# Kernel tuning notes

Hardware: AMD Instinct MI355X
Metric: run time of the kernel (lower is better)

Reference implementation:

```python
import jax, jax.numpy as jnp
import numpy as np

N, E = 50000, 800000
IN, HID, HEADS, OUT = 128, 32, 4, 64
NEG_SLOPE = 0.2
BN_EPS = 1e-5


def setup_inputs() -> dict:
    key = jax.random.key(0)
    ks = jax.random.split(key, 24)
    d1 = HID * HEADS  # 128
    def glorot(k, shape):
        fan = shape[0] + shape[-1]
        return jax.random.uniform(k, shape, jnp.float32, -1.0, 1.0) * jnp.sqrt(6.0 / fan)
    inp = {
        'x': jax.random.normal(ks[0], (N, IN), jnp.float32),
        'edge_index': jax.random.randint(ks[1], (2, E), 0, N, jnp.int64),
        # layer 1: in -> hid x heads
        'W1': glorot(ks[2], (IN, d1)),
        'as1': glorot(ks[3], (HEADS, HID)),
        'ad1': glorot(ks[4], (HEADS, HID)),
        'b1': jnp.zeros((d1,), jnp.float32),
        'g1': jnp.ones((d1,), jnp.float32),
        'be1': jnp.zeros((d1,), jnp.float32),
        # layer 2: d1 -> hid x heads
        'W2': glorot(ks[5], (d1, d1)),
        'as2': glorot(ks[6], (HEADS, HID)),
        'ad2': glorot(ks[7], (HEADS, HID)),
        'b2': jnp.zeros((d1,), jnp.float32),
        'g2': jnp.ones((d1,), jnp.float32),
        'be2': jnp.zeros((d1,), jnp.float32),
        # layer 3: d1 -> out, heads=1, concat=False
        'W3': glorot(ks[8], (d1, OUT)),
        'as3': glorot(ks[9], (1, OUT)),
        'ad3': glorot(ks[10], (1, OUT)),
        'b3': jnp.zeros((OUT,), jnp.float32),
        'g3': jnp.ones((OUT,), jnp.float32),
        'be3': jnp.zeros((OUT,), jnp.float32),
    }
    return inp


def gat_conv(x, src, dst, W, a_s, a_d, b, heads, ch, concat):
    n = x.shape[0]
    h = (x @ W).reshape(n, heads, ch)                       # [N,H,C]
    al_s = jnp.sum(h * a_s, axis=-1)                        # [N,H]
    al_d = jnp.sum(h * a_d, axis=-1)                        # [N,H]
    e = jax.nn.leaky_relu(al_s[src] + al_d[dst], NEG_SLOPE)  # [E,H]
    m = jax.ops.segment_max(e, dst, num_segments=n)
    m = jnp.where(jnp.isfinite(m), m, 0.0)
    ex = jnp.exp(e - m[dst])
    denom = jax.ops.segment_sum(ex, dst, num_segments=n)
    alpha = ex / (denom[dst] + 1e-16)                       # segment softmax
    out = jax.ops.segment_sum(h[src] * alpha[:, :, None], dst, num_segments=n)
    out = out.reshape(n, heads * ch) if concat else out.mean(axis=1)
    return out + b


def batch_norm(x, g, b):
    mu = x.mean(axis=0)
    var = x.var(axis=0)
    return (x - mu) * jax.lax.rsqrt(var + BN_EPS) * g + b


def reference(x, edge_index, W1, as1, ad1, b1, g1, be1,
              W2, as2, ad2, b2, g2, be2,
              W3, as3, ad3, b3, g3, be3):
    n = x.shape[0]
    loops = jnp.arange(n, dtype=edge_index.dtype)
    src = jnp.concatenate([edge_index[0], loops])  # add_self_loops=True
    dst = jnp.concatenate([edge_index[1], loops])
    h = gat_conv(x, src, dst, W1, as1, ad1, b1, HEADS, HID, True)
    h = jax.nn.elu(batch_norm(h, g1, be1))
    h = gat_conv(h, src, dst, W2, as2, ad2, b2, HEADS, HID, True)
    h = jax.nn.elu(batch_norm(h, g2, be2))
    h = gat_conv(h, src, dst, W3, as3, ad3, b3, 1, OUT, False)
    h = jax.nn.elu(batch_norm(h, g3, be3))
    return h
```

## Files before the change

### kernel.cpp

```cpp
#include <hip/hip_runtime.h>
#include <hip/hip_bf16.h>
#include <math.h>

#define NEG_SLOPE 0.2f
#define BN_EPS 1e-5f

using short8_t = __attribute__((ext_vector_type(8))) short;
using f32x4    = __attribute__((ext_vector_type(4))) float;

__device__ __forceinline__ unsigned short f2bf(float f) {
    unsigned int u = __float_as_uint(f);
    u += 0x7FFF + ((u >> 16) & 1);
    return (unsigned short)(u >> 16);
}
__device__ __forceinline__ float bf2f(unsigned short h) {
    return __uint_as_float(((unsigned int)h) << 16);
}


__device__ __forceinline__ void wfrag_one(const float* __restrict__ W,
                                          unsigned short* __restrict__ Wf,
                                          int idx, int D)
{
    int CS = D / 32;
    int i    = idx & 7;
    int lane = (idx >> 3) & 63;
    int f    = idx >> 9;
    int ks   = f & 3;
    int cs   = (f >> 2) % CS;
    int wc   = (f >> 2) / CS;
    int k = ks * 32 + ((lane >> 4) << 3) + i;
    int d = wc * (D / 2) + cs * 16 + (lane & 15);
    Wf[idx] = f2bf(W[k * D + d]);
}

__global__ void setup_all(const float* __restrict__ W1, const float* __restrict__ W2,
                          const float* __restrict__ W3,
                          unsigned short* __restrict__ wf1, unsigned short* __restrict__ wf2,
                          unsigned short* __restrict__ wf3,
                          int* __restrict__ count, int N)
{
    int total = 16384 + 16384 + 8192 + N;
    int st = gridDim.x * blockDim.x;
    for (int idx = blockIdx.x * blockDim.x + threadIdx.x; idx < total; idx += st) {
        if (idx < 16384)       wfrag_one(W1, wf1, idx, 128);
        else if (idx < 32768)  wfrag_one(W2, wf2, idx - 16384, 128);
        else if (idx < 40960)  wfrag_one(W3, wf3, idx - 32768, 64);
        else                   count[idx - 40960] = 0;
    }
}


__global__ void dst_count(const int* __restrict__ ei, int E, int N,
                          int* __restrict__ count, int* __restrict__ ord)
{
    long long total = (long long)E + N;
    long long st = (long long)gridDim.x * blockDim.x;
    for (long long e = (long long)blockIdx.x * blockDim.x + threadIdx.x; e < total; e += st) {
        int dt = (e < E) ? ei[E + e] : (int)(e - E);
        ord[e] = atomicAdd(&count[dt], 1);
    }
}

__global__ void block_sum(const int* __restrict__ count, int* __restrict__ bsum, int N)
{
    __shared__ int sh[256];
    int b = blockIdx.x, t = threadIdx.x;
    int base = b * 1024;
    int s = 0;
    for (int i = t; i < 1024; i += 256) {
        int j = base + i;
        if (j < N) s += count[j];
    }
    sh[t] = s;
    __syncthreads();
    for (int off = 128; off > 0; off >>= 1) {
        if (t < off) sh[t] += sh[t + off];
        __syncthreads();
    }
    if (t == 0) bsum[b] = sh[0];
}

__global__ void scan_bsum(int* __restrict__ bsum, int nb, int* __restrict__ rowptr, int N, int total)
{
    __shared__ int sh[256];
    int t = threadIdx.x;
    sh[t] = (t < nb) ? bsum[t] : 0;
    __syncthreads();
    for (int off = 1; off < 256; off <<= 1) {
        int u = (t >= off) ? sh[t - off] : 0;
        __syncthreads();
        sh[t] += u;
        __syncthreads();
    }
    if (t < nb) bsum[t] = (t == 0) ? 0 : sh[t - 1];
    if (t == 0) rowptr[N] = total;
}

__global__ void scan_final(const int* __restrict__ count, const int* __restrict__ boff,
                           int* __restrict__ rowptr, int N)
{
    __shared__ int sh[256];
    int b = blockIdx.x, t = threadIdx.x;
    int base = b * 1024 + t * 4;
    int c[4];
    int s = 0;
    #pragma unroll
    for (int i = 0; i < 4; ++i) {
        int j = base + i;
        c[i] = (j < N) ? count[j] : 0;
        s += c[i];
    }
    sh[t] = s;
    __syncthreads();
    for (int off = 1; off < 256; off <<= 1) {
        int u = (t >= off) ? sh[t - off] : 0;
        __syncthreads();
        sh[t] += u;
        __syncthreads();
    }
    int run = boff[b] + ((t == 0) ? 0 : sh[t - 1]);
    #pragma unroll
    for (int i = 0; i < 4; ++i) {
        int j = base + i;
        if (j < N) rowptr[j] = run;
        run += c[i];
    }
}

__global__ void csr_scatter(const int* __restrict__ ei, int E, int N,
                            const int* __restrict__ rowptr, const int* __restrict__ ord,
                            int* __restrict__ srcs)
{
    long long total = (long long)E + N;
    long long st = (long long)gridDim.x * blockDim.x;
    for (long long e = (long long)blockIdx.x * blockDim.x + threadIdx.x; e < total; e += st) {
        int s, dt;
        if (e < E) { s = ei[e]; dt = ei[E + e]; }
        else       { s = dt = (int)(e - E); }
        srcs[rowptr[dt] + ord[e]] = s;
    }
}


template<int D, int H, bool BN>
__global__ __launch_bounds__(256, 4) void gemm_mfma(
        const float* __restrict__ x, const unsigned short* __restrict__ Wf,
        const float* __restrict__ colstats, const float* __restrict__ g,
        const float* __restrict__ be,
        const float* __restrict__ a_s, const float* __restrict__ a_d,
        unsigned short* __restrict__ hbuf,
        float* __restrict__ als, float* __restrict__ ald,
        int N, float invN)
{
    constexpr int CS = D / 32;
    __shared__ unsigned short xs[32 * 136];
    __shared__ float affA[128], affB[128];
    __shared__ float red2[4][4][4][2];
    int tid = threadIdx.x, lane = tid & 63, w = tid >> 6;
    int wr = w >> 1, wc = w & 1;
    int n0 = blockIdx.x * 32;

    short8_t bfr[CS][4];
    #pragma unroll
    for (int cs = 0; cs < CS; ++cs)
        #pragma unroll
        for (int ks = 0; ks < 4; ++ks)
            bfr[cs][ks] = *(const short8_t*)(Wf + (((wc * CS + cs) * 4 + ks) << 9) + (lane << 3));

    if (BN) {
        if (tid < 128) {
            float cs_ = colstats[tid], cq = colstats[tid + 128];
            float mu = cs_ * invN;
            float var = cq * invN - mu * mu;
            float s = rsqrtf(var + BN_EPS) * g[tid];
            affA[tid] = s;
            affB[tid] = be[tid] - mu * s;
        }
        __syncthreads();
    }

    for (int jj = tid; jj < 32 * 32; jj += 256) {
        int r = jj >> 5, q = jj & 31;
        float4 v = make_float4(0.f, 0.f, 0.f, 0.f);
        if (n0 + r < N) v = *(const float4*)(x + (long long)(n0 + r) * 128 + q * 4);
        if (BN) {
            int c = q * 4;
            v.x = affA[c]     * v.x + affB[c];
            v.y = affA[c + 1] * v.y + affB[c + 1];
            v.z = affA[c + 2] * v.z + affB[c + 2];
            v.w = affA[c + 3] * v.w + affB[c + 3];
            v.x = (v.x > 0.f) ? v.x : expm1f(v.x);
            v.y = (v.y > 0.f) ? v.y : expm1f(v.y);
            v.z = (v.z > 0.f) ? v.z : expm1f(v.z);
            v.w = (v.w > 0.f) ? v.w : expm1f(v.w);
        }
        ushort4 o;
        o.x = f2bf(v.x); o.y = f2bf(v.y); o.z = f2bf(v.z); o.w = f2bf(v.w);
        *(ushort4*)(xs + r * 136 + q * 4) = o;
    }
    __syncthreads();

    f32x4 acc[CS];
    #pragma unroll
    for (int cs = 0; cs < CS; ++cs) acc[cs] = (f32x4){0.f, 0.f, 0.f, 0.f};

    #pragma unroll
    for (int ks = 0; ks < 4; ++ks) {
        short8_t a = *(const short8_t*)(xs + (wr * 16 + (lane & 15)) * 136
                                           + ks * 32 + ((lane >> 4) << 3));
        #pragma unroll
        for (int cs = 0; cs < CS; ++cs)
            acc[cs] = __builtin_amdgcn_mfma_f32_16x16x32_bf16(a, bfr[cs][ks], acc[cs], 0, 0, 0);
    }

    int mrow = wr * 16 + ((lane >> 4) << 2);
    int dcol = wc * (D / 2) + (lane & 15);
    #pragma unroll
    for (int cs = 0; cs < CS; ++cs)
        #pragma unroll
        for (int r = 0; r < 4; ++r) {
            int n = n0 + mrow + r;
            if (n < N) hbuf[(long long)n * D + dcol + cs * 16] = f2bf(acc[cs][r]);
        }

    int l15 = lane & 15;
    if (H == 4) {
        float ps[2][4], pd[2][4];
        #pragma unroll
        for (int ch = 0; ch < 2; ++ch) {
            int hh = wc * 2 + ch;
            #pragma unroll
            for (int r = 0; r < 4; ++r) { ps[ch][r] = 0.f; pd[ch][r] = 0.f; }
            #pragma unroll
            for (int k2 = 0; k2 < 2; ++k2) {
                int cs = ch * 2 + k2;
                int cih = k2 * 16 + l15;
                float as_v = a_s[hh * 32 + cih];
                float ad_v = a_d[hh * 32 + cih];
                #pragma unroll
                for (int r = 0; r < 4; ++r) {
                    ps[ch][r] += acc[cs][r] * as_v;
                    pd[ch][r] += acc[cs][r] * ad_v;
                }
            }
        }
        #pragma unroll
        for (int off = 1; off < 16; off <<= 1)
            #pragma unroll
            for (int ch = 0; ch < 2; ++ch)
                #pragma unroll
                for (int r = 0; r < 4; ++r) {
                    ps[ch][r] += __shfl_xor(ps[ch][r], off);
                    pd[ch][r] += __shfl_xor(pd[ch][r], off);
                }
        if (l15 == 0) {
            #pragma unroll
            for (int r = 0; r < 4; ++r) {
                int n = n0 + mrow + r;
                if (n < N) {
                    #pragma unroll
                    for (int ch = 0; ch < 2; ++ch) {
                        als[(long long)n * 4 + wc * 2 + ch] = ps[ch][r];
                        ald[(long long)n * 4 + wc * 2 + ch] = pd[ch][r];
                    }
                }
            }
        }
    } else {
        float ps[4], pd[4];
        #pragma unroll
        for (int r = 0; r < 4; ++r) { ps[r] = 0.f; pd[r] = 0.f; }
        #pragma unroll
        for (int cs = 0; cs < CS; ++cs) {
            int c = wc * 32 + cs * 16 + l15;
            float as_v = a_s[c], ad_v = a_d[c];
            #pragma unroll
            for (int r = 0; r < 4; ++r) {
                ps[r] += acc[cs][r] * as_v;
                pd[r] += acc[cs][r] * ad_v;
            }
        }
        #pragma unroll
        for (int off = 1; off < 16; off <<= 1)
            #pragma unroll
            for (int r = 0; r < 4; ++r) {
                ps[r] += __shfl_xor(ps[r], off);
                pd[r] += __shfl_xor(pd[r], off);
            }
        int q = lane >> 4;
        if (l15 == 0) {
            #pragma unroll
            for (int r = 0; r < 4; ++r) {
                red2[w][q][r][0] = ps[r];
                red2[w][q][r][1] = pd[r];
            }
        }
        __syncthreads();
        if (tid < 64) {
            int wr2 = tid >> 5, row = (tid >> 1) & 15, sd = tid & 1;
            int qq = row >> 2, rr = row & 3;
            float v = red2[wr2 * 2][qq][rr][sd] + red2[wr2 * 2 + 1][qq][rr][sd];
            int n = n0 + wr2 * 16 + row;
            if (n < N) { if (sd) ald[n] = v; else als[n] = v; }
        }
    }
}

template<int H, int C>
__global__ __launch_bounds__(256) void gat_aggregate_v5(
        const int* __restrict__ rowptr, const int* __restrict__ srcs,
        const float* __restrict__ als, const float* __restrict__ ald,
        const unsigned short* __restrict__ hbuf, float* __restrict__ agg,
        float* __restrict__ part, int N)
{
    constexpr int D = H * C;
    constexpr int TPN = D / 8;
    constexpr int NPB = 256 / TPN;
    __shared__ float red[4][TPN * 16];
    int tid = threadIdx.x;
    int g = tid / TPN, l = tid % TPN;
    int n = blockIdx.x * NPB + g;
    bool active = (n < N);
    int c0 = l * 8;
    int hh = c0 / C;
    float aldv = active ? ald[(long long)n * H + hh] : 0.f;
    int beg = 0, end = 0;
    if (active) { beg = rowptr[n]; end = rowptr[n + 1]; }

    float wsum = 0.f;
    float acc[8];
    #pragma unroll
    for (int i = 0; i < 8; ++i) acc[i] = 0.f;

    int e = beg;
    for (; e + 4 <= end; e += 4) {
        int s0 = srcs[e], s1 = srcs[e + 1], s2 = srcs[e + 2], s3 = srcs[e + 3];
        float v0 = als[(long long)s0 * H + hh] + aldv;
        float v1 = als[(long long)s1 * H + hh] + aldv;
        float v2 = als[(long long)s2 * H + hh] + aldv;
        float v3 = als[(long long)s3 * H + hh] + aldv;
        v0 = (v0 >= 0.f) ? v0 : NEG_SLOPE * v0;
        v1 = (v1 >= 0.f) ? v1 : NEG_SLOPE * v1;
        v2 = (v2 >= 0.f) ? v2 : NEG_SLOPE * v2;
        v3 = (v3 >= 0.f) ? v3 : NEG_SLOPE * v3;
        float w0 = __expf(v0), w1 = __expf(v1), w2 = __expf(v2), w3 = __expf(v3);
        float4 q0 = *(const float4*)(hbuf + (long long)s0 * D + c0);
        float4 q1 = *(const float4*)(hbuf + (long long)s1 * D + c0);
        float4 q2 = *(const float4*)(hbuf + (long long)s2 * D + c0);
        float4 q3 = *(const float4*)(hbuf + (long long)s3 * D + c0);
        wsum += w0 + w1 + w2 + w3;
        const float* qf0 = (const float*)&q0;
        const float* qf1 = (const float*)&q1;
        const float* qf2 = (const float*)&q2;
        const float* qf3 = (const float*)&q3;
        #pragma unroll
        for (int i = 0; i < 4; ++i) {
            unsigned int u0 = __float_as_uint(qf0[i]);
            unsigned int u1 = __float_as_uint(qf1[i]);
            unsigned int u2 = __float_as_uint(qf2[i]);
            unsigned int u3 = __float_as_uint(qf3[i]);
            acc[2*i]   += w0 * __uint_as_float(u0 << 16)
                        + w1 * __uint_as_float(u1 << 16)
                        + w2 * __uint_as_float(u2 << 16)
                        + w3 * __uint_as_float(u3 << 16);
            acc[2*i+1] += w0 * __uint_as_float(u0 & 0xFFFF0000u)
                        + w1 * __uint_as_float(u1 & 0xFFFF0000u)
                        + w2 * __uint_as_float(u2 & 0xFFFF0000u)
                        + w3 * __uint_as_float(u3 & 0xFFFF0000u);
        }
    }
    for (; e < end; ++e) {
        int s = srcs[e];
        float v = als[(long long)s * H + hh] + aldv;
        v = (v >= 0.f) ? v : NEG_SLOPE * v;
        float w = __expf(v);
        float4 q = *(const float4*)(hbuf + (long long)s * D + c0);
        const float* qf = (const float*)&q;
        wsum += w;
        #pragma unroll
        for (int i = 0; i < 4; ++i) {
            unsigned int u = __float_as_uint(qf[i]);
            acc[2*i]   += w * __uint_as_float(u << 16);
            acc[2*i+1] += w * __uint_as_float(u & 0xFFFF0000u);
        }
    }
    float inv = active ? 1.f / (wsum + 1e-16f) : 0.f;
    float sv[16];
    #pragma unroll
    for (int i = 0; i < 8; ++i) {
        float o = acc[i] * inv;
        sv[i] = o;
        sv[8 + i] = o * o;
        acc[i] = o;
    }
    if (active) {
        *(float4*)(agg + (long long)n * D + c0)     = make_float4(acc[0], acc[1], acc[2], acc[3]);
        *(float4*)(agg + (long long)n * D + c0 + 4) = make_float4(acc[4], acc[5], acc[6], acc[7]);
    }

    #pragma unroll
    for (int off = TPN; off < 64; off <<= 1)
        #pragma unroll
        for (int j = 0; j < 16; ++j)
            sv[j] += __shfl_xor(sv[j], off);

    int w4 = tid >> 6, lane = tid & 63;
    if (lane < TPN) {
        #pragma unroll
        for (int j = 0; j < 16; ++j) red[w4][lane * 16 + j] = sv[j];
    }
    __syncthreads();
    if (w4 == 0 && lane < TPN) {
        #pragma unroll
        for (int ww = 1; ww < 4; ++ww)
            #pragma unroll
            for (int j = 0; j < 16; ++j) sv[j] += red[ww][lane * 16 + j];
        float* p = part + (long long)blockIdx.x * (2 * D) + lane * 16;
        *(float4*)(p)      = make_float4(sv[0],  sv[1],  sv[2],  sv[3]);
        *(float4*)(p + 4)  = make_float4(sv[4],  sv[5],  sv[6],  sv[7]);
        *(float4*)(p + 8)  = make_float4(sv[8],  sv[9],  sv[10], sv[11]);
        *(float4*)(p + 12) = make_float4(sv[12], sv[13], sv[14], sv[15]);
    }
}

template<int D>
__global__ __launch_bounds__(256) void reduce_stats(
        const float* __restrict__ part, int nblk, float* __restrict__ colsum)
{
    __shared__ float sh[256];
    int f = blockIdx.x;
    int t = threadIdx.x;
    int col = (f < D) ? f : (f - D);
    int off = (col / 8) * 16 + (col % 8) + ((f < D) ? 0 : 8);
    float s = 0.f;
    for (int i = t; i < nblk; i += 256)
        s += part[(long long)i * (2 * D) + off];
    sh[t] = s;
    __syncthreads();
    for (int o = 128; o > 0; o >>= 1) {
        if (t < o) sh[t] += sh[t + o];
        __syncthreads();
    }
    if (t == 0) colsum[(f < D) ? f : (128 + f - D)] = sh[0];
}

template<int D>
__global__ __launch_bounds__(256) void bn_apply_v2(
        const float* __restrict__ agg, const float* __restrict__ colsum,
        const float* __restrict__ g, const float* __restrict__ be,
        float* __restrict__ out, int N, float invN)
{
    constexpr int TPR = D / 4;
    constexpr int RPB = 256 / TPR;
    __shared__ float affA[D], affB[D];
    int tid = threadIdx.x;
    if (tid < D) {
        float mu = colsum[tid] * invN;
        float var = colsum[128 + tid] * invN - mu * mu;
        float s = rsqrtf(var + BN_EPS) * g[tid];
        affA[tid] = s;
        affB[tid] = be[tid] - mu * s;
    }
    __syncthreads();
    int rg = tid / TPR, cl = tid % TPR;
    int c = cl * 4;
    float a0 = affA[c], a1 = affA[c+1], a2 = affA[c+2], a3 = affA[c+3];
    float b0 = affB[c], b1 = affB[c+1], b2 = affB[c+2], b3 = affB[c+3];
    for (int r = blockIdx.x * RPB + rg; r < N; r += gridDim.x * RPB) {
        float4 v = *(const float4*)(agg + (long long)r * D + c);
        v.x = a0 * v.x + b0; v.y = a1 * v.y + b1;
        v.z = a2 * v.z + b2; v.w = a3 * v.w + b3;
        v.x = (v.x > 0.f) ? v.x : expm1f(v.x);
        v.y = (v.y > 0.f) ? v.y : expm1f(v.y);
        v.z = (v.z > 0.f) ? v.z : expm1f(v.z);
        v.w = (v.w > 0.f) ? v.w : expm1f(v.w);
        *(float4*)(out + (long long)r * D + c) = v;
    }
}

template<int H, int C, bool BN>
static void run_layer(const float* xin, int N,
                      const int* rowptr, const int* srcs,
                      const unsigned short* Wf, const float* a_s, const float* a_d,
                      const float* prev_stats, const float* prev_g, const float* prev_be,
                      unsigned short* hbuf, float* als, float* ald,
                      float* part, float* stats_out, float* agg,
                      hipStream_t stream)
{
    constexpr int D = H * C;
    constexpr int NPB = 256 / (D / 8);
    int nblk = (N + NPB - 1) / NPB;
    float invN = 1.f / (float)N;
    gemm_mfma<D, H, BN><<<(N + 31) / 32, 256, 0, stream>>>(
        xin, Wf, prev_stats, prev_g, prev_be, a_s, a_d, hbuf, als, ald, N, invN);
    gat_aggregate_v5<H, C><<<nblk, 256, 0, stream>>>(
        rowptr, srcs, als, ald, hbuf, agg, part, N);
    reduce_stats<D><<<2 * D, 256, 0, stream>>>(part, nblk, stats_out);
}

extern "C" void kernel_launch(void* const* d_in, const int* in_sizes, int n_in,
                              void* d_out, int out_size, void* d_ws, size_t ws_size,
                              hipStream_t stream)
{
    const float* x   = (const float*)d_in[0];
    const int*   ei  = (const int*)d_in[1];
    const float* W1  = (const float*)d_in[2];
    const float* as1 = (const float*)d_in[3];
    const float* ad1 = (const float*)d_in[4];
    const float* g1  = (const float*)d_in[6];
    const float* be1 = (const float*)d_in[7];
    const float* W2  = (const float*)d_in[8];
    const float* as2 = (const float*)d_in[9];
    const float* ad2 = (const float*)d_in[10];
    const float* g2  = (const float*)d_in[12];
    const float* be2 = (const float*)d_in[13];
    const float* W3  = (const float*)d_in[14];
    const float* as3 = (const float*)d_in[15];
    const float* ad3 = (const float*)d_in[16];
    const float* g3  = (const float*)d_in[18];
    const float* be3 = (const float*)d_in[19];

    const int N = in_sizes[0] / 128;
    const int E = in_sizes[1] / 2;
    const int NB = (N + 1023) / 1024;

    float* ws   = (float*)d_ws;
    float* aggA = ws;
    float* aggB = aggA + (long long)N * 128;
    float* als  = aggB + (long long)N * 128;
    float* ald  = als  + (long long)N * 4;
    float* cs0  = ald  + (long long)N * 4;
    float* cs1  = cs0 + 256;
    float* cs2  = cs1 + 256;
    unsigned short* hbuf = (unsigned short*)(cs2 + 256);
    int*   rowptr = (int*)(hbuf + (long long)N * 128);
    int*   count  = rowptr + (N + 1);
    int*   bsum   = count + N;
    int*   ord    = bsum + 256;
    int*   srcs   = ord + ((long long)E + N);
    unsigned short* wf1 = (unsigned short*)(srcs + ((long long)E + N));
    unsigned short* wf2 = wf1 + 128 * 128;
    unsigned short* wf3 = wf2 + 128 * 128;
    float* part = (float*)(wf3 + 128 * 64);

    setup_all<<<356, 256, 0, stream>>>(W1, W2, W3, wf1, wf2, wf3, count, N);

    dst_count<<<2048, 256, 0, stream>>>(ei, E, N, count, ord);
    block_sum<<<NB, 256, 0, stream>>>(count, bsum, N);
    scan_bsum<<<1, 256, 0, stream>>>(bsum, NB, rowptr, N, E + N);
    scan_final<<<NB, 256, 0, stream>>>(count, bsum, rowptr, N);
    csr_scatter<<<2048, 256, 0, stream>>>(ei, E, N, rowptr, ord, srcs);

    run_layer<4, 32, false>(x, N, rowptr, srcs, wf1, as1, ad1,
                            nullptr, nullptr, nullptr,
                            hbuf, als, ald, part, cs0, aggA, stream);
    run_layer<4, 32, true>(aggA, N, rowptr, srcs, wf2, as2, ad2,
                           cs0, g1, be1,
                           hbuf, als, ald, part, cs1, aggB, stream);
    run_layer<1, 64, true>(aggB, N, rowptr, srcs, wf3, as3, ad3,
                           cs1, g2, be2,
                           hbuf, als, ald, part, cs2, aggA, stream);
    bn_apply_v2<64><<<2048, 256, 0, stream>>>(aggA, cs2, g3, be3, (float*)d_out, N, 1.f / (float)N);
}
```

Baseline: 227.3 us.

## Sort destination nodes by degree to balance aggregation workload per block

Adds a counting-sort pass (histogram, scan, scatter) that builds a permutation of nodes ordered by in-degree, and makes the aggregation kernel process nodes via this permutation. Nodes with similar degree then share a block, which is meant to reduce intra-block imbalance and wavefront divergence in the edge loop. In exchange it adds three small kernel launches, an extra indirection per node, and scattered (non-contiguous) writes of agg rows and node reads.

```diff
diff --git a/kernel.cpp b/kernel.cpp
--- a/kernel.cpp
+++ b/kernel.cpp
@@ -4,6 +4,7 @@
 
 #define NEG_SLOPE 0.2f
 #define BN_EPS 1e-5f
+#define NBH 64
 
 using short8_t = __attribute__((ext_vector_type(8))) short;
 using f32x4    = __attribute__((ext_vector_type(4))) float;
@@ -139,6 +140,62 @@
         if (e < E) { s = ei[e]; dt = ei[E + e]; }
         else       { s = dt = (int)(e - E); }
         srcs[rowptr[dt] + ord[e]] = s;
+    }
+}
+
+
+__global__ void deg_hist(const int* __restrict__ count, int N, int chunk,
+                         int* __restrict__ hist)
+{
+    __shared__ int h[256];
+    int b = blockIdx.x, t = threadIdx.x;
+    h[t] = 0;
+    __syncthreads();
+    int lo = b * chunk, hi = min(N, lo + chunk);
+    for (int i = lo + t; i < hi; i += 256) {
+        int d = count[i]; if (d > 255) d = 255;
+        atomicAdd(&h[d], 1);
+    }
+    __syncthreads();
+    hist[b * 256 + t] = h[t];
+}
+
+__global__ void deg_scan(const int* __restrict__ hist, int* __restrict__ blockBase)
+{
+    __shared__ int tot[256];
+    int t = threadIdx.x;
+    int s = 0;
+    for (int b = 0; b < NBH; ++b) s += hist[b * 256 + t];
+    int v = s;
+    tot[t] = s;
+    __syncthreads();
+    for (int off = 1; off < 256; off <<= 1) {
+        int u = (t >= off) ? tot[t - off] : 0;
+        __syncthreads();
+        tot[t] += u;
+        __syncthreads();
+    }
+    int run = tot[t] - v;
+    for (int b = 0; b < NBH; ++b) {
+        blockBase[b * 256 + t] = run;
+        run += hist[b * 256 + t];
+    }
+}
+
+__global__ void perm_scatter(const int* __restrict__ count, int N, int chunk,
+                             const int* __restrict__ blockBase, int* __restrict__ perm)
+{
+    __shared__ int h[256];
+    __shared__ int bb[256];
+    int b = blockIdx.x, t = threadIdx.x;
+    h[t] = 0;
+    bb[t] = blockBase[b * 256 + t];
+    __syncthreads();
+    int lo = b * chunk, hi = min(N, lo + chunk);
+    for (int i = lo + t; i < hi; i += 256) {
+        int d = count[i]; if (d > 255) d = 255;
+        int lr = atomicAdd(&h[d], 1);
+        perm[bb[d] + lr] = i;
     }
 }
 
@@ -308,7 +365,8 @@
 }
 
 template<int H, int C>
-__global__ __launch_bounds__(256) void gat_aggregate_v5(
+__global__ __launch_bounds__(256) void gat_aggregate_v6(
+        const int* __restrict__ perm,
         const int* __restrict__ rowptr, const int* __restrict__ srcs,
         const float* __restrict__ als, const float* __restrict__ ald,
         const unsigned short* __restrict__ hbuf, float* __restrict__ agg,
@@ -320,8 +378,9 @@
     __shared__ float red[4][TPN * 16];
     int tid = threadIdx.x;
     int g = tid / TPN, l = tid % TPN;
-    int n = blockIdx.x * NPB + g;
-    bool active = (n < N);
+    int idx = blockIdx.x * NPB + g;
+    bool active = (idx < N);
+    int n = active ? perm[idx] : 0;
     int c0 = l * 8;
     int hh = c0 / C;
     float aldv = active ? ald[(long long)n * H + hh] : 0.f;
@@ -481,7 +540,7 @@
 
 template<int H, int C, bool BN>
 static void run_layer(const float* xin, int N,
-                      const int* rowptr, const int* srcs,
+                      const int* perm, const int* rowptr, const int* srcs,
                       const unsigned short* Wf, const float* a_s, const float* a_d,
                       const float* prev_stats, const float* prev_g, const float* prev_be,
                       unsigned short* hbuf, float* als, float* ald,
@@ -494,8 +553,8 @@
     float invN = 1.f / (float)N;
     gemm_mfma<D, H, BN><<<(N + 31) / 32, 256, 0, stream>>>(
         xin, Wf, prev_stats, prev_g, prev_be, a_s, a_d, hbuf, als, ald, N, invN);
-    gat_aggregate_v5<H, C><<<nblk, 256, 0, stream>>>(
-        rowptr, srcs, als, ald, hbuf, agg, part, N);
+    gat_aggregate_v6<H, C><<<nblk, 256, 0, stream>>>(
+        perm, rowptr, srcs, als, ald, hbuf, agg, part, N);
     reduce_stats<D><<<2 * D, 256, 0, stream>>>(part, nblk, stats_out);
 }
 
@@ -524,6 +583,7 @@
     const int N = in_sizes[0] / 128;
     const int E = in_sizes[1] / 2;
     const int NB = (N + 1023) / 1024;
+    const int CHUNK = (N + NBH - 1) / NBH;
 
     float* ws   = (float*)d_ws;
     float* aggA = ws;
@@ -543,6 +603,9 @@
     unsigned short* wf2 = wf1 + 128 * 128;
     unsigned short* wf3 = wf2 + 128 * 128;
     float* part = (float*)(wf3 + 128 * 64);
+    int*   hist = (int*)(part + ((long long)(N + 15) / 16) * 256);
+    int*   bbase = hist + NBH * 256;
+    int*   perm  = bbase + NBH * 256;
 
     setup_all<<<356, 256, 0, stream>>>(W1, W2, W3, wf1, wf2, wf3, count, N);
 
@@ -552,13 +615,17 @@
     scan_final<<<NB, 256, 0, stream>>>(count, bsum, rowptr, N);
     csr_scatter<<<2048, 256, 0, stream>>>(ei, E, N, rowptr, ord, srcs);
 
-    run_layer<4, 32, false>(x, N, rowptr, srcs, wf1, as1, ad1,
+    deg_hist<<<NBH, 256, 0, stream>>>(count, N, CHUNK, hist);
+    deg_scan<<<1, 256, 0, stream>>>(hist, bbase);
+    perm_scatter<<<NBH, 256, 0, stream>>>(count, N, CHUNK, bbase, perm);
+
+    run_layer<4, 32, false>(x, N, perm, rowptr, srcs, wf1, as1, ad1,
                             nullptr, nullptr, nullptr,
                             hbuf, als, ald, part, cs0, aggA, stream);
-    run_layer<4, 32, true>(aggA, N, rowptr, srcs, wf2, as2, ad2,
+    run_layer<4, 32, true>(aggA, N, perm, rowptr, srcs, wf2, as2, ad2,
                            cs0, g1, be1,
                            hbuf, als, ald, part, cs1, aggB, stream);
-    run_layer<1, 64, true>(aggB, N, rowptr, srcs, wf3, as3, ad3,
+    run_layer<1, 64, true>(aggB, N, perm, rowptr, srcs, wf3, as3, ad3,
                            cs1, g2, be2,
                            hbuf, als, ald, part, cs2, aggA, stream);
     bn_apply_v2<64><<<2048, 256, 0, stream>>>(aggA, cs2, g3, be3, (float*)d_out, N, 1.f / (float)N);
```

Result: slower. 242.1 us (+6.5%).
